# Kernel optimization log

Measured on AMD Instinct MI355X. Metric: run time of the kernel, lower is better.

## Reference

```python
import jax, jax.numpy as jnp
import numpy as np

B, L, D = 8, 8192, 128
H, C = 2, 64          # heads, out_channels = dim // 2; H*C == D so the final view works
N = B * L
E = 1048576
NEG_SLOPE = 0.2


def setup_inputs() -> dict:
    key = jax.random.key(0)
    k1, k2, k3, k4, k5 = jax.random.split(key, 5)
    x = jax.random.normal(k1, (B, L, D), dtype=jnp.float32)
    edge_index = jax.random.randint(k2, (2, E), 0, N, dtype=jnp.int64)
    s = 1.0 / np.sqrt(D)
    W_l = jax.random.uniform(k3, (D, H * C), minval=-s, maxval=s, dtype=jnp.float32)
    W_r = jax.random.uniform(k4, (D, H * C), minval=-s, maxval=s, dtype=jnp.float32)
    att = jax.random.uniform(k5, (H, C), minval=-s, maxval=s, dtype=jnp.float32)
    bias = jnp.zeros((H * C,), dtype=jnp.float32)
    return {"x": x, "edge_index": edge_index, "W_l": W_l, "W_r": W_r, "att": att, "bias": bias}


def reference(x, edge_index, W_l, W_r, att, bias):
    # x: [B, L, D] -> flatten to node features [N, D]
    xf = x.reshape(N, D)
    x_l = (xf @ W_l).reshape(N, H, C)  # source transform
    x_r = (xf @ W_r).reshape(N, H, C)  # target transform

    # add self loops (PyG GATv2Conv default add_self_loops=True)
    loops = jnp.arange(N, dtype=edge_index.dtype)
    src = jnp.concatenate([edge_index[0], loops])  # [E+N]
    dst = jnp.concatenate([edge_index[1], loops])

    # GATv2 attention: e_ij = att . LeakyReLU(x_l[j] + x_r[i])
    feat = jax.nn.leaky_relu(x_l[src] + x_r[dst], NEG_SLOPE)  # [E+N, H, C]
    score = jnp.einsum('ehc,hc->eh', feat, att)               # [E+N, H]

    # segment softmax over incoming edges of each target node
    m = jax.ops.segment_max(score, dst, num_segments=N)       # [N, H]
    num = jnp.exp(score - m[dst])
    den = jax.ops.segment_sum(num, dst, num_segments=N)       # [N, H]
    alpha = num / den[dst]                                    # [E+N, H]

    # weighted aggregation of transformed source features
    out = jax.ops.segment_sum(alpha[:, :, None] * x_l[src], dst, num_segments=N)  # [N, H, C]
    out = out.reshape(N, H * C) + bias
    return out.reshape(B, L, D)
```

## Files before the change

kernel.cpp:

```cpp
#include <hip/hip_runtime.h>

typedef unsigned short u16;
typedef unsigned int   u32;

#define NN     65536
#define DDIM   128
#define EE     1048576
#define NEG_SLOPE 0.2f
#define SUBCAP 640
#define BROW   8192

typedef __attribute__((ext_vector_type(8))) short          short8;
typedef __attribute__((ext_vector_type(2))) float          f32x2;
typedef __attribute__((ext_vector_type(4))) float          f32x4;
typedef __attribute__((ext_vector_type(4))) u32            u32x4;

__device__ __forceinline__ float bf2f(u16 b) { return __uint_as_float(((u32)b) << 16); }
__device__ __forceinline__ u16 f2bf(float f) {
  u32 u = __float_as_uint(f);
  u += 0x7FFFu + ((u >> 16) & 1u);
  return (u16)(u >> 16);
}
__device__ __forceinline__ f32x2 bfp2f(u32 w) {
  f32x2 r;
  r.x = __uint_as_float(w << 16);
  r.y = __uint_as_float(w & 0xFFFF0000u);
  return r;
}
__device__ __forceinline__ f32x2 pk_max(f32x2 a, f32x2 b) {
  f32x2 r; r.x = fmaxf(a.x, b.x); r.y = fmaxf(a.y, b.y); return r;
}

__global__ void init_misc(const int* __restrict__ ei, u32* __restrict__ mode,
                          const float* __restrict__ Wl, const float* __restrict__ Wr,
                          u16* __restrict__ wpack, u32* __restrict__ cursor) {
  int t = threadIdx.x, b = blockIdx.x;
  if (b == 0) {
    if (t < 64) {
      int nz = (ei[2 * t + 1] != 0) ? 1 : 0;
      unsigned long long bal = __ballot(nz);
      if (t == 0) mode[0] = (bal == 0ull) ? 1u : 0u;
    }
    return;
  }
  if (b <= 8) {
    int pb = b - 1;
    int colhalf = pb >> 2, ks = pb & 3;
    int lane = t & 63, pp = t >> 6;
    int m16 = lane & 15, quad = lane >> 4;
#pragma unroll
    for (int pq = 0; pq < 2; ++pq) {
      int p = pq * 4 + pp;
      const float* W = (p < 4) ? Wl : Wr;
      int n = colhalf * 64 + (p & 3) * 16 + m16;
#pragma unroll
      for (int j = 0; j < 8; ++j) {
        int k = ks * 32 + quad * 8 + j;
        wpack[(((((colhalf * 4 + ks) * 8) + p) * 64 + lane) * 8) + j] = f2bf(W[k * DDIM + n]);
      }
    }
    return;
  }
  int i = (b - 9) * 256 + t;
#pragma unroll
  for (int k = 0; k < 16; ++k) cursor[i * 16 + k] = 0;
}

__device__ __forceinline__ void gemm_body(
    int pb, int tid,
    const float* __restrict__ x, const u16* __restrict__ wpack,
    u16* __restrict__ xl, u16* __restrict__ xr)
{
  int wave = tid >> 6;
  int lane = tid & 63;
  int m16  = lane & 15;
  int quad = lane >> 4;
  int mat     = wave >> 1;
  int colhalf = wave & 1;
  int rowbase = pb * 64;

  const u16* wp = wpack + (size_t)colhalf * (4 * 8 * 64 * 8);
  short8 bfr[4][4];
#pragma unroll
  for (int ks = 0; ks < 4; ++ks)
#pragma unroll
    for (int ct = 0; ct < 4; ++ct)
      bfr[ks][ct] = *(const short8*)(wp + ((size_t)(ks * 8 + mat * 4 + ct) * 64 + lane) * 8);

  u16* outp = mat ? xr : xl;
#pragma unroll
  for (int rt = 0; rt < 4; ++rt) {
    int r0 = rowbase + rt * 16;
    f32x4 acc[4] = { {0,0,0,0},{0,0,0,0},{0,0,0,0},{0,0,0,0} };
#pragma unroll
    for (int ks = 0; ks < 4; ++ks) {
      const float* ap = x + (size_t)(r0 + m16) * DDIM + ks * 32 + quad * 8;
      f32x4 a0 = *(const f32x4*)ap;
      f32x4 a1 = *(const f32x4*)(ap + 4);
      short8 a;
#pragma unroll
      for (int c = 0; c < 4; ++c) { a[c] = (short)f2bf(a0[c]); a[4 + c] = (short)f2bf(a1[c]); }
#pragma unroll
      for (int ct = 0; ct < 4; ++ct)
        acc[ct] = __builtin_amdgcn_mfma_f32_16x16x32_bf16(a, bfr[ks][ct], acc[ct], 0, 0, 0);
    }
#pragma unroll
    for (int ct = 0; ct < 4; ++ct) {
      int c = colhalf * 64 + ct * 16 + m16;
#pragma unroll
      for (int rg = 0; rg < 4; ++rg) {
        int r = r0 + quad * 4 + rg;
        outp[(size_t)r * DDIM + c] = f2bf(acc[ct][rg]);
      }
    }
  }
}

__device__ __forceinline__ void pass1_body(
    int pb, int t,
    const int* __restrict__ ei, u32* __restrict__ cursor,
    u32* __restrict__ subb, const u32* __restrict__ mode,
    u32* lcnt, u32* gb)
{
  lcnt[t] = 0;
  __syncthreads();

  int base = (pb * 256 + t) * 8;
  int s[8], d[8];
  if (mode[0]) {
    const long long* ei64 = (const long long*)ei;
#pragma unroll
    for (int k = 0; k < 4; ++k) {
      longlong2 sv = *(const longlong2*)(ei64 + base + 2 * k);
      longlong2 dv = *(const longlong2*)(ei64 + EE + base + 2 * k);
      s[2 * k] = (int)sv.x; s[2 * k + 1] = (int)sv.y;
      d[2 * k] = (int)dv.x; d[2 * k + 1] = (int)dv.y;
    }
  } else {
#pragma unroll
    for (int k = 0; k < 2; ++k) {
      int4 sv = *(const int4*)(ei + base + 4 * k);
      int4 dv = *(const int4*)(ei + EE + base + 4 * k);
      s[4 * k] = sv.x; s[4 * k + 1] = sv.y; s[4 * k + 2] = sv.z; s[4 * k + 3] = sv.w;
      d[4 * k] = dv.x; d[4 * k + 1] = dv.y; d[4 * k + 2] = dv.z; d[4 * k + 3] = dv.w;
    }
  }

  u32 rk[8];
#pragma unroll
  for (int e = 0; e < 8; ++e)
    rk[e] = atomicAdd(&lcnt[(u32)d[e] >> 8], 1u);
  __syncthreads();

  int xs = pb & 7;
  gb[t] = atomicAdd(&cursor[(t * 8 + xs) * 16], lcnt[t]);
  __syncthreads();

#pragma unroll
  for (int e = 0; e < 8; ++e) {
    u32 cell = (u32)d[e] >> 8;
    u32 pos  = gb[cell] + rk[e];
    if (pos < SUBCAP)
      subb[(size_t)(cell * 8 + xs) * SUBCAP + pos] =
          ((u32)(d[e] & 255) << 16) | (u32)s[e];
  }
}

__global__ __launch_bounds__(256) void gemm_pass1(
    const float* __restrict__ x, const u16* __restrict__ wpack,
    u16* __restrict__ xl, u16* __restrict__ xr,
    const int* __restrict__ ei, u32* __restrict__ cursor,
    u32* __restrict__ subb, const u32* __restrict__ mode)
{
  __shared__ u32 lcnt[256];
  __shared__ u32 gb[256];
  int b = blockIdx.x;
  if (b < 1024) gemm_body(b, threadIdx.x, x, wpack, xl, xr);
  else          pass1_body(b - 1024, threadIdx.x, ei, cursor, subb, mode, lcnt, gb);
}

__global__ __launch_bounds__(1024) void pass2_build(const u32* __restrict__ cursor,
                                                    const u32* __restrict__ subb,
                                                    u32* __restrict__ rowptr,
                                                    u16* __restrict__ csr,
                                                    u32* __restrict__ perm)
{
  __shared__ u32 sh[256];
  __shared__ u32 cnt[256];
  __shared__ u32 cbase[256];
  __shared__ u32 hist[64];
  int b = blockIdx.x, t = threadIdx.x;

  if (t < 256) { cnt[t] = 0; if (t < 64) hist[t] = 0; }
  __syncthreads();

  u32 sizes[8];
#pragma unroll
  for (int x = 0; x < 8; ++x) sizes[x] = min(cursor[(b * 8 + x) * 16], (u32)SUBCAP);

  u32 ent[8], rk[8];
  bool has[8];
#pragma unroll
  for (int x = 0; x < 8; ++x) {
    has[x] = ((u32)t < sizes[x]);
    ent[x] = 0; rk[x] = 0;
    if (has[x]) {
      u32 e = subb[(size_t)(b * 8 + x) * SUBCAP + t];
      ent[x] = e;
      rk[x]  = atomicAdd(&cnt[e >> 16], 1u);
    }
  }
  __syncthreads();

  u32 c = 0, dc = 0, pc = 0;
  if (t < 256) {
    c  = cnt[t];
    dc = min(c, 63u);
    pc = (c + 7u) & ~7u;
    atomicAdd(&hist[dc], 1u);
    sh[t] = pc;
  }
  __syncthreads();
  for (int off = 1; off < 256; off <<= 1) {
    u32 v = 0, a = 0;
    if (t < 256) { v = sh[t]; a = (t >= off) ? sh[t - off] : 0u; }
    __syncthreads();
    if (t < 256) sh[t] = v + a;
    __syncthreads();
  }
  if (t < 256) {
    u32 loc = sh[t] - pc;
    cbase[t] = loc;
    rowptr[b * 256 + t] = ((b * BROW + loc) << 8) | c;
  }
  __syncthreads();
  if (t == 0) {
    u32 run = 0;
    for (int i = 0; i < 64; ++i) { u32 h = hist[i]; hist[i] = run; run += h; }
  }
  __syncthreads();
  if (t < 256) {
    u32 r = atomicAdd(&hist[dc], 1u);
    perm[b * 256 + r] = b * 256 + t;
  }
  __syncthreads();

#pragma unroll
  for (int x = 0; x < 8; ++x) {
    if (has[x]) {
      u32 cell = ent[x] >> 16;
      csr[b * BROW + cbase[cell] + rk[x]] = (u16)(ent[x] & 0xFFFFu);
    }
  }
}

__device__ __forceinline__ void gat_item(u32x4 xw, const f32x2* av, const f32x2* rv,
                                         float& l, f32x2* acc)
{
  f32x2 xv[4];
  f32x2 sc2 = {0.f, 0.f};
#pragma unroll
  for (int i = 0; i < 4; ++i) {
    xv[i] = bfp2f(xw[i]);
    f32x2 t = xv[i] + rv[i];
    f32x2 lr = pk_max(t, t * NEG_SLOPE);
    sc2 += av[i] * lr;
  }
  float partial = sc2.x + sc2.y;
  partial += __shfl_xor(partial, 1);
  partial += __shfl_xor(partial, 2);
  partial += __shfl_xor(partial, 4);
  float p = __expf(partial);
  l += p;
#pragma unroll
  for (int i = 0; i < 4; ++i) acc[i] += p * xv[i];
}

__global__ __launch_bounds__(256) void gat_fused(
    const u16* __restrict__ xl, const u16* __restrict__ xr,
    const u32* __restrict__ rowptr, const u16* __restrict__ csr,
    const u32* __restrict__ perm,
    const float* __restrict__ att, const float* __restrict__ bias,
    float* __restrict__ out)
{
  int tid    = threadIdx.x;
  int bucket = blockIdx.x & 255;
  int tier   = blockIdx.x >> 8;
  int node   = (int)perm[bucket * 256 + (15 - tier) * 16 + (tid >> 4)];
  int q      = tid & 15;
  int c0     = q * 8;
  const u16* __restrict__ xlc = xl + c0;

  u32x4 SW = *(const u32x4*)(xlc + (size_t)node * DDIM);

  f32x2 av[4], rv[4];
  {
    f32x4 a0 = *(const f32x4*)(att + c0);
    f32x4 a1 = *(const f32x4*)(att + c0 + 4);
    av[0].x = a0[0]; av[0].y = a0[1]; av[1].x = a0[2]; av[1].y = a0[3];
    av[2].x = a1[0]; av[2].y = a1[1]; av[3].x = a1[2]; av[3].y = a1[3];
    u32x4 rw = *(const u32x4*)(xr + (size_t)node * DDIM + c0);
#pragma unroll
    for (int i = 0; i < 4; ++i) rv[i] = bfp2f(rw[i]);
  }

  float l = 0.f;
  f32x2 acc[4] = { {0,0},{0,0},{0,0},{0,0} };

  u32 rp  = rowptr[node];
  u32 rs  = rp >> 8;
  int deg = (int)(rp & 255u);
  const u16* __restrict__ cp = csr + rs;

  gat_item(SW, av, rv, l, acc);

  int j = 0;
  while (deg - j >= 16) {
    u32x4 iw0 = *(const u32x4*)(cp + j);
    u32x4 iw1 = *(const u32x4*)(cp + j + 8);
    u32 i0  = iw0.x & 0xFFFFu, i1  = iw0.x >> 16, i2  = iw0.y & 0xFFFFu, i3  = iw0.y >> 16;
    u32 i4  = iw0.z & 0xFFFFu, i5  = iw0.z >> 16, i6  = iw0.w & 0xFFFFu, i7  = iw0.w >> 16;
    u32 i8  = iw1.x & 0xFFFFu, i9  = iw1.x >> 16, i10 = iw1.y & 0xFFFFu, i11 = iw1.y >> 16;
    u32 i12 = iw1.z & 0xFFFFu, i13 = iw1.z >> 16, i14 = iw1.w & 0xFFFFu, i15 = iw1.w >> 16;
    u32x4 L0  = *(const u32x4*)(xlc + (size_t)i0  * DDIM);
    u32x4 L1  = *(const u32x4*)(xlc + (size_t)i1  * DDIM);
    u32x4 L2  = *(const u32x4*)(xlc + (size_t)i2  * DDIM);
    u32x4 L3  = *(const u32x4*)(xlc + (size_t)i3  * DDIM);
    u32x4 L4  = *(const u32x4*)(xlc + (size_t)i4  * DDIM);
    u32x4 L5  = *(const u32x4*)(xlc + (size_t)i5  * DDIM);
    u32x4 L6  = *(const u32x4*)(xlc + (size_t)i6  * DDIM);
    u32x4 L7  = *(const u32x4*)(xlc + (size_t)i7  * DDIM);
    u32x4 L8  = *(const u32x4*)(xlc + (size_t)i8  * DDIM);
    u32x4 L9  = *(const u32x4*)(xlc + (size_t)i9  * DDIM);
    u32x4 L10 = *(const u32x4*)(xlc + (size_t)i10 * DDIM);
    u32x4 L11 = *(const u32x4*)(xlc + (size_t)i11 * DDIM);
    u32x4 L12 = *(const u32x4*)(xlc + (size_t)i12 * DDIM);
    u32x4 L13 = *(const u32x4*)(xlc + (size_t)i13 * DDIM);
    u32x4 L14 = *(const u32x4*)(xlc + (size_t)i14 * DDIM);
    u32x4 L15 = *(const u32x4*)(xlc + (size_t)i15 * DDIM);
    __builtin_amdgcn_sched_barrier(0);
    gat_item(L0,  av, rv, l, acc);
    gat_item(L1,  av, rv, l, acc);
    gat_item(L2,  av, rv, l, acc);
    gat_item(L3,  av, rv, l, acc);
    gat_item(L4,  av, rv, l, acc);
    gat_item(L5,  av, rv, l, acc);
    gat_item(L6,  av, rv, l, acc);
    gat_item(L7,  av, rv, l, acc);
    gat_item(L8,  av, rv, l, acc);
    gat_item(L9,  av, rv, l, acc);
    gat_item(L10, av, rv, l, acc);
    gat_item(L11, av, rv, l, acc);
    gat_item(L12, av, rv, l, acc);
    gat_item(L13, av, rv, l, acc);
    gat_item(L14, av, rv, l, acc);
    gat_item(L15, av, rv, l, acc);
    j += 16;
  }
  if (deg - j >= 8) {
    u32x4 iw = *(const u32x4*)(cp + j);
    u32 i0 = iw.x & 0xFFFFu, i1 = iw.x >> 16, i2 = iw.y & 0xFFFFu, i3 = iw.y >> 16;
    u32 i4 = iw.z & 0xFFFFu, i5 = iw.z >> 16, i6 = iw.w & 0xFFFFu, i7 = iw.w >> 16;
    u32x4 L0 = *(const u32x4*)(xlc + (size_t)i0 * DDIM);
    u32x4 L1 = *(const u32x4*)(xlc + (size_t)i1 * DDIM);
    u32x4 L2 = *(const u32x4*)(xlc + (size_t)i2 * DDIM);
    u32x4 L3 = *(const u32x4*)(xlc + (size_t)i3 * DDIM);
    u32x4 L4 = *(const u32x4*)(xlc + (size_t)i4 * DDIM);
    u32x4 L5 = *(const u32x4*)(xlc + (size_t)i5 * DDIM);
    u32x4 L6 = *(const u32x4*)(xlc + (size_t)i6 * DDIM);
    u32x4 L7 = *(const u32x4*)(xlc + (size_t)i7 * DDIM);
    __builtin_amdgcn_sched_barrier(0);
    gat_item(L0, av, rv, l, acc);
    gat_item(L1, av, rv, l, acc);
    gat_item(L2, av, rv, l, acc);
    gat_item(L3, av, rv, l, acc);
    gat_item(L4, av, rv, l, acc);
    gat_item(L5, av, rv, l, acc);
    gat_item(L6, av, rv, l, acc);
    gat_item(L7, av, rv, l, acc);
    j += 8;
  }
  if (deg - j >= 4) {
    uint2 iw = *(const uint2*)(cp + j);
    u32 i0 = iw.x & 0xFFFFu, i1 = iw.x >> 16, i2 = iw.y & 0xFFFFu, i3 = iw.y >> 16;
    u32x4 L0 = *(const u32x4*)(xlc + (size_t)i0 * DDIM);
    u32x4 L1 = *(const u32x4*)(xlc + (size_t)i1 * DDIM);
    u32x4 L2 = *(const u32x4*)(xlc + (size_t)i2 * DDIM);
    u32x4 L3 = *(const u32x4*)(xlc + (size_t)i3 * DDIM);
    __builtin_amdgcn_sched_barrier(0);
    gat_item(L0, av, rv, l, acc);
    gat_item(L1, av, rv, l, acc);
    gat_item(L2, av, rv, l, acc);
    gat_item(L3, av, rv, l, acc);
    j += 4;
  }
  for (; j < deg; ++j) {
    u32 s = cp[j];
    u32x4 xw = *(const u32x4*)(xlc + (size_t)s * DDIM);
    gat_item(xw, av, rv, l, acc);
  }

  float inv = 1.f / l;
  f32x4 o0, o1;
  o0[0] = fmaf(acc[0].x, inv, bias[c0 + 0]);
  o0[1] = fmaf(acc[0].y, inv, bias[c0 + 1]);
  o0[2] = fmaf(acc[1].x, inv, bias[c0 + 2]);
  o0[3] = fmaf(acc[1].y, inv, bias[c0 + 3]);
  o1[0] = fmaf(acc[2].x, inv, bias[c0 + 4]);
  o1[1] = fmaf(acc[2].y, inv, bias[c0 + 5]);
  o1[2] = fmaf(acc[3].x, inv, bias[c0 + 6]);
  o1[3] = fmaf(acc[3].y, inv, bias[c0 + 7]);
  float* op = out + (size_t)node * DDIM + c0;
  *(f32x4*)op       = o0;
  *(f32x4*)(op + 4) = o1;
}

extern "C" void kernel_launch(void* const* d_in, const int* in_sizes, int n_in,
                              void* d_out, int out_size, void* d_ws, size_t ws_size,
                              hipStream_t stream) {
  (void)in_sizes; (void)n_in; (void)out_size; (void)ws_size;
  const float* x    = (const float*)d_in[0];
  const int*   ei   = (const int*)d_in[1];
  const float* Wl   = (const float*)d_in[2];
  const float* Wr   = (const float*)d_in[3];
  const float* attw = (const float*)d_in[4];
  const float* bias = (const float*)d_in[5];
  float* out = (float*)d_out;

  char* w = (char*)d_ws;
  u16* xl     = (u16*)(w);
  u16* xr     = (u16*)(w + (16u << 20));
  u32* subb   = (u32*)(w + (32u << 20));
  u32* cursor = (u32*)(w + (37u << 20));
  u32* mode   = (u32*)(w + (37u << 20) + (192u << 10));
  u32* rowptr = (u32*)(w + (37u << 20) + (256u << 10));
  u16* csr    = (u16*)(w + (37u << 20) + (512u << 10));
  u16* wpack  = (u16*)(w + (41u << 20) + (512u << 10));
  u32* perm   = (u32*)(w + (41u << 20) + (640u << 10));

  init_misc<<<17, 256, 0, stream>>>(ei, mode, Wl, Wr, wpack, cursor);
  gemm_pass1<<<1536, 256, 0, stream>>>(x, wpack, xl, xr, ei, cursor, subb, mode);
  pass2_build<<<256, 1024, 0, stream>>>(cursor, subb, rowptr, csr, perm);
  gat_fused<<<NN / 16, 256, 0, stream>>>(xl, xr, rowptr, csr, perm, attw, bias, out);
}
```

Measured before the change: 176.3 us.

## Fuse GEMM with CSR build and rebalance node-to-wave assignment in GAT kernel

Edge binning now runs as its own kernel, and the dense projection GEMM is co-scheduled with the per-bucket CSR build instead of with binning. The CSR build now uses 256-thread blocks that process three entries per thread rather than 1024-thread blocks. The GAT kernel assigns nodes to waves from degree-sorted groups in a mirrored pattern, pairing low- and high-degree groups in each block to balance work across blocks. This hides the build phase behind GEMM work. The cost is an extra dependency, since binning must finish before the GEMM launch, and higher register use for the buffered entries.

```diff
diff --git a/kernel.cpp b/kernel.cpp
--- a/kernel.cpp
+++ b/kernel.cpp
@@ -66,6 +66,58 @@
   for (int k = 0; k < 16; ++k) cursor[i * 16 + k] = 0;
 }
 
+__global__ __launch_bounds__(256) void pass1_bin(const int* __restrict__ ei,
+                                                 u32* __restrict__ cursor,
+                                                 u32* __restrict__ subb,
+                                                 const u32* __restrict__ mode)
+{
+  __shared__ u32 lcnt[256];
+  __shared__ u32 gb[256];
+  int pb = blockIdx.x, t = threadIdx.x;
+  lcnt[t] = 0;
+  __syncthreads();
+
+  int base = (pb * 256 + t) * 8;
+  int s[8], d[8];
+  if (mode[0]) {
+    const long long* ei64 = (const long long*)ei;
+#pragma unroll
+    for (int k = 0; k < 4; ++k) {
+      longlong2 sv = *(const longlong2*)(ei64 + base + 2 * k);
+      longlong2 dv = *(const longlong2*)(ei64 + EE + base + 2 * k);
+      s[2 * k] = (int)sv.x; s[2 * k + 1] = (int)sv.y;
+      d[2 * k] = (int)dv.x; d[2 * k + 1] = (int)dv.y;
+    }
+  } else {
+#pragma unroll
+    for (int k = 0; k < 2; ++k) {
+      int4 sv = *(const int4*)(ei + base + 4 * k);
+      int4 dv = *(const int4*)(ei + EE + base + 4 * k);
+      s[4 * k] = sv.x; s[4 * k + 1] = sv.y; s[4 * k + 2] = sv.z; s[4 * k + 3] = sv.w;
+      d[4 * k] = dv.x; d[4 * k + 1] = dv.y; d[4 * k + 2] = dv.z; d[4 * k + 3] = dv.w;
+    }
+  }
+
+  u32 rk[8];
+#pragma unroll
+  for (int e = 0; e < 8; ++e)
+    rk[e] = atomicAdd(&lcnt[(u32)d[e] >> 8], 1u);
+  __syncthreads();
+
+  int xs = pb & 7;
+  gb[t] = atomicAdd(&cursor[(t * 8 + xs) * 16], lcnt[t]);
+  __syncthreads();
+
+#pragma unroll
+  for (int e = 0; e < 8; ++e) {
+    u32 cell = (u32)d[e] >> 8;
+    u32 pos  = gb[cell] + rk[e];
+    if (pos < SUBCAP)
+      subb[(size_t)(cell * 8 + xs) * SUBCAP + pos] =
+          ((u32)(d[e] & 255) << 16) | (u32)s[e];
+  }
+}
+
 __device__ __forceinline__ void gemm_body(
     int pb, int tid,
     const float* __restrict__ x, const u16* __restrict__ wpack,
@@ -116,142 +168,84 @@
   }
 }
 
-__device__ __forceinline__ void pass1_body(
-    int pb, int t,
-    const int* __restrict__ ei, u32* __restrict__ cursor,
-    u32* __restrict__ subb, const u32* __restrict__ mode,
-    u32* lcnt, u32* gb)
-{
-  lcnt[t] = 0;
-  __syncthreads();
-
-  int base = (pb * 256 + t) * 8;
-  int s[8], d[8];
-  if (mode[0]) {
-    const long long* ei64 = (const long long*)ei;
-#pragma unroll
-    for (int k = 0; k < 4; ++k) {
-      longlong2 sv = *(const longlong2*)(ei64 + base + 2 * k);
-      longlong2 dv = *(const longlong2*)(ei64 + EE + base + 2 * k);
-      s[2 * k] = (int)sv.x; s[2 * k + 1] = (int)sv.y;
-      d[2 * k] = (int)dv.x; d[2 * k + 1] = (int)dv.y;
-    }
-  } else {
-#pragma unroll
-    for (int k = 0; k < 2; ++k) {
-      int4 sv = *(const int4*)(ei + base + 4 * k);
-      int4 dv = *(const int4*)(ei + EE + base + 4 * k);
-      s[4 * k] = sv.x; s[4 * k + 1] = sv.y; s[4 * k + 2] = sv.z; s[4 * k + 3] = sv.w;
-      d[4 * k] = dv.x; d[4 * k + 1] = dv.y; d[4 * k + 2] = dv.z; d[4 * k + 3] = dv.w;
-    }
-  }
-
-  u32 rk[8];
-#pragma unroll
-  for (int e = 0; e < 8; ++e)
-    rk[e] = atomicAdd(&lcnt[(u32)d[e] >> 8], 1u);
-  __syncthreads();
-
-  int xs = pb & 7;
-  gb[t] = atomicAdd(&cursor[(t * 8 + xs) * 16], lcnt[t]);
-  __syncthreads();
-
-#pragma unroll
-  for (int e = 0; e < 8; ++e) {
-    u32 cell = (u32)d[e] >> 8;
-    u32 pos  = gb[cell] + rk[e];
-    if (pos < SUBCAP)
-      subb[(size_t)(cell * 8 + xs) * SUBCAP + pos] =
-          ((u32)(d[e] & 255) << 16) | (u32)s[e];
-  }
-}
-
-__global__ __launch_bounds__(256) void gemm_pass1(
+__device__ __forceinline__ void pass2_body(
+    int b, int t,
+    const u32* __restrict__ cursor, const u32* __restrict__ subb,
+    u32* __restrict__ rowptr, u16* __restrict__ csr, u32* __restrict__ perm,
+    u32* sh, u32* cnt, u32* cbase, u32* hist)
+{
+  cnt[t] = 0;
+  if (t < 64) hist[t] = 0;
+  __syncthreads();
+
+  u32 sizes[8];
+#pragma unroll
+  for (int x = 0; x < 8; ++x) sizes[x] = min(cursor[(b * 8 + x) * 16], (u32)SUBCAP);
+
+  u32 ent[8][3], rk[8][3];
+#pragma unroll
+  for (int x = 0; x < 8; ++x) {
+    const u32* sp = subb + (size_t)(b * 8 + x) * SUBCAP;
+#pragma unroll
+    for (int r = 0; r < 3; ++r) {
+      u32 i = (u32)t + r * 256u;
+      ent[x][r] = 0xFFFFFFFFu; rk[x][r] = 0;
+      if (i < sizes[x]) {
+        u32 e = sp[i];
+        ent[x][r] = e;
+        rk[x][r]  = atomicAdd(&cnt[e >> 16], 1u);
+      }
+    }
+  }
+  __syncthreads();
+
+  u32 c  = cnt[t];
+  u32 dc = min(c, 63u);
+  u32 pc = (c + 7u) & ~7u;
+  atomicAdd(&hist[dc], 1u);
+  sh[t] = pc;
+  __syncthreads();
+  for (int off = 1; off < 256; off <<= 1) {
+    u32 v = sh[t]; u32 a = (t >= off) ? sh[t - off] : 0u;
+    __syncthreads(); sh[t] = v + a; __syncthreads();
+  }
+  u32 loc = sh[t] - pc;
+  cbase[t] = loc;
+  rowptr[b * 256 + t] = ((b * BROW + loc) << 8) | min(c, 255u);
+  __syncthreads();
+  if (t == 0) {
+    u32 run = 0;
+    for (int i = 0; i < 64; ++i) { u32 h = hist[i]; hist[i] = run; run += h; }
+  }
+  __syncthreads();
+  u32 r2 = atomicAdd(&hist[dc], 1u);
+  perm[b * 256 + r2] = b * 256 + t;
+  __syncthreads();
+
+#pragma unroll
+  for (int x = 0; x < 8; ++x)
+#pragma unroll
+    for (int r = 0; r < 3; ++r)
+      if (ent[x][r] != 0xFFFFFFFFu) {
+        u32 cell = ent[x][r] >> 16;
+        csr[b * BROW + cbase[cell] + rk[x][r]] = (u16)(ent[x][r] & 0xFFFFu);
+      }
+}
+
+__global__ __launch_bounds__(256) void gemm_pass2(
     const float* __restrict__ x, const u16* __restrict__ wpack,
     u16* __restrict__ xl, u16* __restrict__ xr,
-    const int* __restrict__ ei, u32* __restrict__ cursor,
-    u32* __restrict__ subb, const u32* __restrict__ mode)
-{
-  __shared__ u32 lcnt[256];
-  __shared__ u32 gb[256];
-  int b = blockIdx.x;
-  if (b < 1024) gemm_body(b, threadIdx.x, x, wpack, xl, xr);
-  else          pass1_body(b - 1024, threadIdx.x, ei, cursor, subb, mode, lcnt, gb);
-}
-
-__global__ __launch_bounds__(1024) void pass2_build(const u32* __restrict__ cursor,
-                                                    const u32* __restrict__ subb,
-                                                    u32* __restrict__ rowptr,
-                                                    u16* __restrict__ csr,
-                                                    u32* __restrict__ perm)
+    const u32* __restrict__ cursor, const u32* __restrict__ subb,
+    u32* __restrict__ rowptr, u16* __restrict__ csr, u32* __restrict__ perm)
 {
   __shared__ u32 sh[256];
   __shared__ u32 cnt[256];
   __shared__ u32 cbase[256];
   __shared__ u32 hist[64];
-  int b = blockIdx.x, t = threadIdx.x;
-
-  if (t < 256) { cnt[t] = 0; if (t < 64) hist[t] = 0; }
-  __syncthreads();
-
-  u32 sizes[8];
-#pragma unroll
-  for (int x = 0; x < 8; ++x) sizes[x] = min(cursor[(b * 8 + x) * 16], (u32)SUBCAP);
-
-  u32 ent[8], rk[8];
-  bool has[8];
-#pragma unroll
-  for (int x = 0; x < 8; ++x) {
-    has[x] = ((u32)t < sizes[x]);
-    ent[x] = 0; rk[x] = 0;
-    if (has[x]) {
-      u32 e = subb[(size_t)(b * 8 + x) * SUBCAP + t];
-      ent[x] = e;
-      rk[x]  = atomicAdd(&cnt[e >> 16], 1u);
-    }
-  }
-  __syncthreads();
-
-  u32 c = 0, dc = 0, pc = 0;
-  if (t < 256) {
-    c  = cnt[t];
-    dc = min(c, 63u);
-    pc = (c + 7u) & ~7u;
-    atomicAdd(&hist[dc], 1u);
-    sh[t] = pc;
-  }
-  __syncthreads();
-  for (int off = 1; off < 256; off <<= 1) {
-    u32 v = 0, a = 0;
-    if (t < 256) { v = sh[t]; a = (t >= off) ? sh[t - off] : 0u; }
-    __syncthreads();
-    if (t < 256) sh[t] = v + a;
-    __syncthreads();
-  }
-  if (t < 256) {
-    u32 loc = sh[t] - pc;
-    cbase[t] = loc;
-    rowptr[b * 256 + t] = ((b * BROW + loc) << 8) | c;
-  }
-  __syncthreads();
-  if (t == 0) {
-    u32 run = 0;
-    for (int i = 0; i < 64; ++i) { u32 h = hist[i]; hist[i] = run; run += h; }
-  }
-  __syncthreads();
-  if (t < 256) {
-    u32 r = atomicAdd(&hist[dc], 1u);
-    perm[b * 256 + r] = b * 256 + t;
-  }
-  __syncthreads();
-
-#pragma unroll
-  for (int x = 0; x < 8; ++x) {
-    if (has[x]) {
-      u32 cell = ent[x] >> 16;
-      csr[b * BROW + cbase[cell] + rk[x]] = (u16)(ent[x] & 0xFFFFu);
-    }
-  }
+  int b = blockIdx.x;
+  if (b < 1024) gemm_body(b, threadIdx.x, x, wpack, xl, xr);
+  else          pass2_body(b - 1024, threadIdx.x, cursor, subb,
+                           rowptr, csr, perm, sh, cnt, cbase, hist);
 }
 
 __device__ __forceinline__ void gat_item(u32x4 xw, const f32x2* av, const f32x2* rv,
@@ -285,8 +279,11 @@
 {
   int tid    = threadIdx.x;
   int bucket = blockIdx.x & 255;
-  int tier   = blockIdx.x >> 8;
-  int node   = (int)perm[bucket * 256 + (15 - tier) * 16 + (tid >> 4)];
+  int k      = blockIdx.x >> 8;
+  int wave   = tid >> 6;
+  int wg     = (wave == 0) ? k : (wave == 1) ? (31 - k)
+             : (wave == 2) ? (32 + k) : (63 - k);
+  int node   = (int)perm[bucket * 256 + wg * 4 + ((tid >> 4) & 3)];
   int q      = tid & 15;
   int c0     = q * 8;
   const u16* __restrict__ xlc = xl + c0;
@@ -439,7 +436,8 @@
   u32* perm   = (u32*)(w + (41u << 20) + (640u << 10));
 
   init_misc<<<17, 256, 0, stream>>>(ei, mode, Wl, Wr, wpack, cursor);
-  gemm_pass1<<<1536, 256, 0, stream>>>(x, wpack, xl, xr, ei, cursor, subb, mode);
-  pass2_build<<<256, 1024, 0, stream>>>(cursor, subb, rowptr, csr, perm);
+  pass1_bin<<<512, 256, 0, stream>>>(ei, cursor, subb, mode);
+  gemm_pass2<<<1280, 256, 0, stream>>>(x, wpack, xl, xr, cursor, subb,
+                                       rowptr, csr, perm);
   gat_fused<<<NN / 16, 256, 0, stream>>>(xl, xr, rowptr, csr, perm, attw, bias, out);
 }
```

Measured after the change: 179.7 us. No clear change (+2.0%).
